# Kernel optimization log

Measured on AMD Instinct MI355X. Metric: run time of the kernel, lower is better.

The kernel has to match this reference:

```python
import jax, jax.numpy as jnp
import numpy as np

N_NODES = 50000
N_EDGES = 800000
IN_DIM = 128
HEADS = 4
HID = 32
NEG_SLOPE = 0.2


def setup_inputs() -> dict:
    key = jax.random.key(0)
    ks = jax.random.split(key, 10)

    def glorot(k, shape, fan):
        return jax.random.normal(k, shape, jnp.float32) * (1.0 / np.sqrt(fan))

    x = jax.random.normal(ks[0], (N_NODES, IN_DIM), jnp.float32)
    edge_index = jax.random.randint(ks[1], (2, N_EDGES), 0, N_NODES)
    # layer 1: in=IN_DIM, out=HEADS*HID (concat)
    Wl1 = glorot(ks[2], (IN_DIM, HEADS * HID), IN_DIM)
    Wr1 = glorot(ks[3], (IN_DIM, HEADS * HID), IN_DIM)
    att1 = glorot(ks[4], (HEADS, HID), HID)
    b1 = jnp.zeros((HEADS * HID,), jnp.float32)
    # layer 2: in=HEADS*HID, out=HID (mean over heads)
    Wl2 = glorot(ks[5], (HEADS * HID, HEADS * HID), HEADS * HID)
    Wr2 = glorot(ks[6], (HEADS * HID, HEADS * HID), HEADS * HID)
    att2 = glorot(ks[7], (HEADS, HID), HID)
    b2 = jnp.zeros((HID,), jnp.float32)
    return {"x": x, "edge_index": edge_index, "Wl1": Wl1, "Wr1": Wr1,
            "att1": att1, "b1": b1, "Wl2": Wl2, "Wr2": Wr2,
            "att2": att2, "b2": b2}


def _gatv2_conv(x, src, dst, Wl, Wr, att, bias, concat):
    """PyG GATv2Conv (eval mode, self loops already in src/dst)."""
    n = x.shape[0]
    h, c = att.shape
    xl = (x @ Wl).reshape(n, h, c)  # source transform
    xr = (x @ Wr).reshape(n, h, c)  # destination transform
    e = jax.nn.leaky_relu(xl[src] + xr[dst], NEG_SLOPE)   # [E, H, C]
    logits = jnp.einsum('ehc,hc->eh', e, att)             # [E, H]
    # segment softmax over edges grouped by destination node
    m = jax.ops.segment_max(logits, dst, num_segments=n)  # [N, H]
    a = jnp.exp(logits - m[dst])
    denom = jax.ops.segment_sum(a, dst, num_segments=n)   # [N, H]
    alpha = a / denom[dst]                                # [E, H]
    out = jax.ops.segment_sum(xl[src] * alpha[..., None], dst,
                              num_segments=n)             # [N, H, C]
    out = out.reshape(n, h * c) if concat else out.mean(axis=1)
    return out + bias


def reference(x, edge_index, Wl1, Wr1, att1, b1, Wl2, Wr2, att2, b2):
    n = x.shape[0]
    loop = jnp.arange(n, dtype=edge_index.dtype)
    src = jnp.concatenate([edge_index[0], loop])
    dst = jnp.concatenate([edge_index[1], loop])
    h1 = jax.nn.relu(_gatv2_conv(x, src, dst, Wl1, Wr1, att1, b1, concat=True))
    h2 = jax.nn.relu(_gatv2_conv(h1, src, dst, Wl2, Wr2, att2, b2, concat=False))
    return h2
```

## Files before the change

kernel.cpp:

```cpp
#include <hip/hip_runtime.h>
#include <hip/hip_bf16.h>
#include <hip/hip_fp16.h>

#define HEADS 4
#define HID 32
#define DIM 128
#define CAP 64


typedef __attribute__((ext_vector_type(8))) short bf16x8;
typedef __attribute__((ext_vector_type(4))) float f32x4;

__device__ __forceinline__ float bf2f(unsigned short u) {
    return __uint_as_float(((unsigned int)u) << 16);
}
__device__ __forceinline__ unsigned short f2bf(float f) {
    unsigned int u = __float_as_uint(f);
    unsigned int r = u + 0x7fffu + ((u >> 16) & 1u);
    return (unsigned short)(r >> 16);
}
__device__ __forceinline__ float2 h2f2(unsigned int u) {
    __half2 h = *(__half2*)&u;
    return make_float2(__low2float(h), __high2float(h));
}

__device__ __forceinline__ void wprep_block(int blk,
                      const float* __restrict__ Wl, const float* __restrict__ Wr,
                      uint4* __restrict__ wf)
{
    const int gtid = blk * 256 + threadIdx.x;
    const int lane = gtid & 63;
    const int ks = (gtid >> 6) & 3;
    const int nt = gtid >> 8;
    const int col = nt * 16 + (lane & 15);
    const int kbase = ks * 32 + (lane >> 4) * 8;
    unsigned short hs[8], ls[8];
#pragma unroll
    for (int j = 0; j < 8; ++j) {
        int k = kbase + j;
        float w = (col < 128) ? Wl[(size_t)k * 128 + col] : Wr[(size_t)k * 128 + col - 128];
        hs[j] = f2bf(w);
        ls[j] = f2bf(w - bf2f(hs[j]));
    }
    uint4 H, L;
    H.x = hs[0] | ((unsigned)hs[1] << 16); H.y = hs[2] | ((unsigned)hs[3] << 16);
    H.z = hs[4] | ((unsigned)hs[5] << 16); H.w = hs[6] | ((unsigned)hs[7] << 16);
    L.x = ls[0] | ((unsigned)ls[1] << 16); L.y = ls[2] | ((unsigned)ls[3] << 16);
    L.z = ls[4] | ((unsigned)ls[5] << 16); L.w = ls[6] | ((unsigned)ls[7] << 16);
    wf[((0 * 16 + nt) * 4 + ks) * 64 + lane] = H;
    wf[((1 * 16 + nt) * 4 + ks) * 64 + lane] = L;
}

__global__ void prep(int* __restrict__ cnt, int N, int ZB,
                     const float* __restrict__ Wl1, const float* __restrict__ Wr1,
                     uint4* __restrict__ wf1,
                     const float* __restrict__ Wl2, const float* __restrict__ Wr2,
                     uint4* __restrict__ wf2)
{
    int b = blockIdx.x;
    if (b < ZB) {
        int i = b * 256 + threadIdx.x;
        if (i < N) cnt[i] = 0;
        return;
    }
    b -= ZB;
    if (b < 16) wprep_block(b, Wl1, Wr1, wf1);
    else        wprep_block(b - 16, Wl2, Wr2, wf2);
}

__global__ void scatter_edges(const int* __restrict__ ei, int E,
                              int* __restrict__ cnt, int* __restrict__ bucket)
{
    int e = blockIdx.x * blockDim.x + threadIdx.x;
    if (e < E) {
        int s = ei[e], d = ei[E + e];
        int slot = atomicAdd(&cnt[d], 1);
        if (slot < CAP) bucket[(size_t)d * CAP + slot] = s;
    }
}

__global__ void __launch_bounds__(256, 2)
mfma_gemm(const float* __restrict__ xf, const uint4* __restrict__ wf,
          unsigned short* __restrict__ xlh, float* __restrict__ xr, int N)
{
    const int tid = threadIdx.x;
    const int base = blockIdx.x * 64;
    __shared__ uint4 ldsA[2 * 4 * 4 * 64];

#pragma unroll
    for (int it = 0; it < 4; ++it) {
        int t = tid + it * 256;
        int r = t >> 4, kb = t & 15;
        int row = base + r;
        float v[8];
        if (row < N) {
            size_t idx = (size_t)row * DIM + kb * 8;
            float4 p0 = *(const float4*)(xf + idx);
            float4 p1 = *(const float4*)(xf + idx + 4);
            v[0] = p0.x; v[1] = p0.y; v[2] = p0.z; v[3] = p0.w;
            v[4] = p1.x; v[5] = p1.y; v[6] = p1.z; v[7] = p1.w;
        } else {
#pragma unroll
            for (int j = 0; j < 8; ++j) v[j] = 0.f;
        }
        unsigned short hs[8], ls[8];
#pragma unroll
        for (int j = 0; j < 8; ++j) {
            hs[j] = f2bf(v[j]);
            ls[j] = f2bf(v[j] - bf2f(hs[j]));
        }
        uint4 H, L;
        H.x = hs[0] | ((unsigned)hs[1] << 16); H.y = hs[2] | ((unsigned)hs[3] << 16);
        H.z = hs[4] | ((unsigned)hs[5] << 16); H.w = hs[6] | ((unsigned)hs[7] << 16);
        L.x = ls[0] | ((unsigned)ls[1] << 16); L.y = ls[2] | ((unsigned)ls[3] << 16);
        L.z = ls[4] | ((unsigned)ls[5] << 16); L.w = ls[6] | ((unsigned)ls[7] << 16);
        int mtile = r >> 4, kstep = kb >> 2, lane = (kb & 3) * 16 + (r & 15);
        ldsA[((0 * 4 + mtile) * 4 + kstep) * 64 + lane] = H;
        ldsA[((1 * 4 + mtile) * 4 + kstep) * 64 + lane] = L;
    }
    __syncthreads();

    const int w = tid >> 6, lane = tid & 63;
    const int nloc = lane & 15;
    const int e0 = (lane >> 4) << 2;

#pragma unroll 2
    for (int ntq = 0; ntq < 4; ++ntq) {
        const int nt = w * 4 + ntq;
        bf16x8 bh[4], bl[4];
#pragma unroll
        for (int ks = 0; ks < 4; ++ks) {
            bh[ks] = *(const bf16x8*)&wf[((0 * 16 + nt) * 4 + ks) * 64 + lane];
            bl[ks] = *(const bf16x8*)&wf[((1 * 16 + nt) * 4 + ks) * 64 + lane];
        }
#pragma unroll
        for (int mt = 0; mt < 4; ++mt) {
            f32x4 a0 = {0.f, 0.f, 0.f, 0.f};
            f32x4 a1 = {0.f, 0.f, 0.f, 0.f};
            f32x4 a2 = {0.f, 0.f, 0.f, 0.f};
#pragma unroll
            for (int ks = 0; ks < 4; ++ks) {
                bf16x8 ah = *(bf16x8*)&ldsA[((0 * 4 + mt) * 4 + ks) * 64 + lane];
                bf16x8 al = *(bf16x8*)&ldsA[((1 * 4 + mt) * 4 + ks) * 64 + lane];
                a0 = __builtin_amdgcn_mfma_f32_16x16x32_bf16(ah, bh[ks], a0, 0, 0, 0);
                a1 = __builtin_amdgcn_mfma_f32_16x16x32_bf16(al, bh[ks], a1, 0, 0, 0);
                a2 = __builtin_amdgcn_mfma_f32_16x16x32_bf16(ah, bl[ks], a2, 0, 0, 0);
            }
            f32x4 acc = a0 + a1 + a2;
            const int r0 = base + mt * 16 + e0;
            if (nt < 8) {
                const int col = nt * 16 + nloc;
#pragma unroll
                for (int e = 0; e < 4; ++e) {
                    int row = r0 + e;
                    if (row < N) xlh[(size_t)row * DIM + col] = __half_as_ushort(__float2half(acc[e]));
                }
            } else {
                const int col = nt * 16 + nloc - 128;
#pragma unroll
                for (int e = 0; e < 4; ++e) {
                    int row = r0 + e;
                    if (row < N) xr[(size_t)row * DIM + col] = acc[e];
                }
            }
        }
    }
}

template<int LAYER>
__global__ void fused_node(const unsigned short* __restrict__ xlh, const float* __restrict__ xr,
                           const int* __restrict__ bucket, const int* __restrict__ cnt,
                           const float* __restrict__ att, const float* __restrict__ bias,
                           int N, void* __restrict__ outp)
{
    const int node = blockIdx.x * 4 + (threadIdx.x >> 6);
    if (node >= N) return;
    const int l = threadIdx.x & 63;
    const unsigned int* xl2 = (const unsigned int*)xlh;

    const float att0 = att[2 * l];
    const float att1 = att[2 * l + 1];
    const float2 rv = *(const float2*)(xr + (size_t)node * DIM + 2 * l);

    int deg = cnt[node];
    deg = deg < CAP ? deg : CAP;
    const int m = deg + 1;
    const int* bk = bucket + (size_t)node * CAP;

    const int myslot = (l < deg) ? bk[l] : node;
#define SRCOF(J) ((J) < deg ? __shfl(myslot, (J) & 63) : node)

    unsigned int b[4];
#pragma unroll
    for (int p = 0; p < 4; ++p) b[p] = xl2[(size_t)SRCOF(p) * 64 + l];

    float num0 = 0.f, num1 = 0.f, den = 0.f;
    const int mfull = m & ~3;
    for (int j = 0; j < mfull; j += 4) {
#pragma unroll
        for (int p = 0; p < 4; ++p) {
            float2 v = h2f2(b[p]);
            b[p] = xl2[(size_t)SRCOF(j + 4 + p) * 64 + l];
            float u0 = v.x + rv.x, u1 = v.y + rv.y;
            float t = fmaf(att0, fmaxf(u0, 0.2f * u0),
                           att1 * fmaxf(u1, 0.2f * u1));
#pragma unroll
            for (int off = 1; off < 16; off <<= 1) t += __shfl_xor(t, off);
            float a = __expf(fminf(fmaxf(t, -50.f), 50.f));
            den += a;
            num0 = fmaf(a, v.x, num0);
            num1 = fmaf(a, v.y, num1);
        }
    }
    const int rem = m - mfull;
    if (rem) {
#pragma unroll
        for (int p = 0; p < 4; ++p) {
            if (p < rem) {
                float2 v = h2f2(b[p]);
                float u0 = v.x + rv.x, u1 = v.y + rv.y;
                float t = fmaf(att0, fmaxf(u0, 0.2f * u0),
                               att1 * fmaxf(u1, 0.2f * u1));
#pragma unroll
                for (int off = 1; off < 16; off <<= 1) t += __shfl_xor(t, off);
                float a = __expf(fminf(fmaxf(t, -50.f), 50.f));
                den += a;
                num0 = fmaf(a, v.x, num0);
                num1 = fmaf(a, v.y, num1);
            }
        }
    }
#undef SRCOF
    float o0 = num0 / den, o1 = num1 / den;

    if (LAYER == 1) {
        float w0 = o0 + bias[2 * l];
        float w1 = o1 + bias[2 * l + 1];
        float2 st = make_float2(w0 > 0.f ? w0 : 0.f, w1 > 0.f ? w1 : 0.f);
        *(float2*)((float*)outp + (size_t)node * DIM + 2 * l) = st;
    } else {
        float s0v = o0, s1v = o1;
        s0v += __shfl_xor(s0v, 16); s0v += __shfl_xor(s0v, 32);
        s1v += __shfl_xor(s1v, 16); s1v += __shfl_xor(s1v, 32);
        if (l < 16) {
            float v0 = 0.25f * s0v + bias[2 * l];
            float v1 = 0.25f * s1v + bias[2 * l + 1];
            v0 = v0 > 0.f ? v0 : 0.f;
            v1 = v1 > 0.f ? v1 : 0.f;
            *(float2*)((float*)outp + (size_t)node * HID + 2 * l) = make_float2(v0, v1);
        }
    }
}

extern "C" void kernel_launch(void* const* d_in, const int* in_sizes, int n_in,
                              void* d_out, int out_size, void* d_ws, size_t ws_size,
                              hipStream_t stream)
{
    const float* x   = (const float*)d_in[0];
    const int*   ei  = (const int*)d_in[1];
    const float* Wl1 = (const float*)d_in[2];
    const float* Wr1 = (const float*)d_in[3];
    const float* at1 = (const float*)d_in[4];
    const float* b1  = (const float*)d_in[5];
    const float* Wl2 = (const float*)d_in[6];
    const float* Wr2 = (const float*)d_in[7];
    const float* at2 = (const float*)d_in[8];
    const float* b2  = (const float*)d_in[9];

    const int N = in_sizes[0] / DIM;
    const int E = in_sizes[1] / 2;

    float* ws = (float*)d_ws;
    const size_t NF = (size_t)N * DIM;
    unsigned short* f_xlh = (unsigned short*)ws;
    float* f_xr   = ws + NF / 2;
    float* f_h1   = f_xr + NF;
    int*   bucket = (int*)(f_h1 + NF);
    int*   cnt    = bucket + (size_t)N * CAP;
    size_t wf_off = ((size_t)(cnt + N) - (size_t)d_ws + 15) & ~(size_t)15;
    uint4* wfrag1 = (uint4*)((char*)d_ws + wf_off);
    uint4* wfrag2 = wfrag1 + 8192;

    const dim3 B(256);
    const int gemm_blocks = (N + 63) / 64;
    const int node_blocks = (N + 3) / 4;
    const int ZB = (N + 255) / 256;

    prep<<<ZB + 32, B, 0, stream>>>(cnt, N, ZB, Wl1, Wr1, wfrag1, Wl2, Wr2, wfrag2);
    scatter_edges<<<(E + 255) / 256, B, 0, stream>>>(ei, E, cnt, bucket);

    mfma_gemm<<<gemm_blocks, B, 0, stream>>>(x, wfrag1, f_xlh, f_xr, N);
    fused_node<1><<<node_blocks, B, 0, stream>>>(f_xlh, f_xr, bucket, cnt, at1, b1, N, f_h1);

    mfma_gemm<<<gemm_blocks, B, 0, stream>>>(f_h1, wfrag2, f_xlh, f_xr, N);
    fused_node<2><<<node_blocks, B, 0, stream>>>(f_xlh, f_xr, bucket, cnt, at2, b2, N, d_out);
}
```

Before: 282.0 us.

## Merge edge scatter into layer-1 GEMM launch and simplify leaky-relu attention math

The edge-bucketing scatter kernel is folded into the first GEMM launch as extra blocks, so bucketing runs concurrently with the layer-1 projection and one kernel launch is removed. Separately, the leaky-relu dot product with the attention vector is rewritten as 0.6*a*u + 0.4*a*|u| with precomputed coefficients, which replaces the max operations with fused multiply-adds. The merged kernel carries extra parameters and a branch, and scatter blocks share the register and LDS budget of the GEMM kernel, which may affect occupancy.

```diff
diff --git a/kernel.cpp b/kernel.cpp
--- a/kernel.cpp
+++ b/kernel.cpp
@@ -68,21 +68,22 @@
     else        wprep_block(b - 16, Wl2, Wr2, wf2);
 }
 
-__global__ void scatter_edges(const int* __restrict__ ei, int E,
-                              int* __restrict__ cnt, int* __restrict__ bucket)
-{
-    int e = blockIdx.x * blockDim.x + threadIdx.x;
-    if (e < E) {
-        int s = ei[e], d = ei[E + e];
-        int slot = atomicAdd(&cnt[d], 1);
-        if (slot < CAP) bucket[(size_t)d * CAP + slot] = s;
-    }
-}
-
 __global__ void __launch_bounds__(256, 2)
 mfma_gemm(const float* __restrict__ xf, const uint4* __restrict__ wf,
-          unsigned short* __restrict__ xlh, float* __restrict__ xr, int N)
-{
+          unsigned short* __restrict__ xlh, float* __restrict__ xr, int N,
+          int gemmBlocks, const int* __restrict__ ei, int E,
+          int* __restrict__ cnt, int* __restrict__ bucket)
+{
+    if ((int)blockIdx.x >= gemmBlocks) {
+        int e = ((int)blockIdx.x - gemmBlocks) * 256 + threadIdx.x;
+        if (e < E) {
+            int s = ei[e], d = ei[E + e];
+            int slot = atomicAdd(&cnt[d], 1);
+            if (slot < CAP) bucket[(size_t)d * CAP + slot] = s;
+        }
+        return;
+    }
+
     const int tid = threadIdx.x;
     const int base = blockIdx.x * 64;
     __shared__ uint4 ldsA[2 * 4 * 4 * 64];
@@ -178,8 +179,9 @@
     const int l = threadIdx.x & 63;
     const unsigned int* xl2 = (const unsigned int*)xlh;
 
-    const float att0 = att[2 * l];
-    const float att1 = att[2 * l + 1];
+    const float att0 = att[2 * l], att1 = att[2 * l + 1];
+    const float c0 = 0.6f * att0, c0a = 0.4f * att0;
+    const float c1 = 0.6f * att1, c1a = 0.4f * att1;
     const float2 rv = *(const float2*)(xr + (size_t)node * DIM + 2 * l);
 
     int deg = cnt[node];
@@ -202,8 +204,8 @@
             float2 v = h2f2(b[p]);
             b[p] = xl2[(size_t)SRCOF(j + 4 + p) * 64 + l];
             float u0 = v.x + rv.x, u1 = v.y + rv.y;
-            float t = fmaf(att0, fmaxf(u0, 0.2f * u0),
-                           att1 * fmaxf(u1, 0.2f * u1));
+            float t = fmaf(c0a, fabsf(u0), c0 * u0);
+            t = fmaf(c1a, fabsf(u1), fmaf(c1, u1, t));
 #pragma unroll
             for (int off = 1; off < 16; off <<= 1) t += __shfl_xor(t, off);
             float a = __expf(fminf(fmaxf(t, -50.f), 50.f));
@@ -219,8 +221,8 @@
             if (p < rem) {
                 float2 v = h2f2(b[p]);
                 float u0 = v.x + rv.x, u1 = v.y + rv.y;
-                float t = fmaf(att0, fmaxf(u0, 0.2f * u0),
-                               att1 * fmaxf(u1, 0.2f * u1));
+                float t = fmaf(c0a, fabsf(u0), c0 * u0);
+                t = fmaf(c1a, fabsf(u1), fmaf(c1, u1, t));
 #pragma unroll
                 for (int off = 1; off < 16; off <<= 1) t += __shfl_xor(t, off);
                 float a = __expf(fminf(fmaxf(t, -50.f), 50.f));
@@ -285,13 +287,15 @@
     const int gemm_blocks = (N + 63) / 64;
     const int node_blocks = (N + 3) / 4;
     const int ZB = (N + 255) / 256;
+    const int scat_blocks = (E + 255) / 256;
 
     prep<<<ZB + 32, B, 0, stream>>>(cnt, N, ZB, Wl1, Wr1, wfrag1, Wl2, Wr2, wfrag2);
-    scatter_edges<<<(E + 255) / 256, B, 0, stream>>>(ei, E, cnt, bucket);
-
-    mfma_gemm<<<gemm_blocks, B, 0, stream>>>(x, wfrag1, f_xlh, f_xr, N);
+
+    mfma_gemm<<<gemm_blocks + scat_blocks, B, 0, stream>>>(
+        x, wfrag1, f_xlh, f_xr, N, gemm_blocks, ei, E, cnt, bucket);
     fused_node<1><<<node_blocks, B, 0, stream>>>(f_xlh, f_xr, bucket, cnt, at1, b1, N, f_h1);
 
-    mfma_gemm<<<gemm_blocks, B, 0, stream>>>(f_h1, wfrag2, f_xlh, f_xr, N);
+    mfma_gemm<<<gemm_blocks, B, 0, stream>>>(
+        f_h1, wfrag2, f_xlh, f_xr, N, gemm_blocks, nullptr, 0, nullptr, nullptr);
     fused_node<2><<<node_blocks, B, 0, stream>>>(f_xlh, f_xr, bucket, cnt, at2, b2, N, d_out);
 }
```

After: 283.4 us. No clear change (+0.5%).
